# Optimization experiments

Measured on AMD Instinct MI355X. Metric: run time of the kernel, lower is better.

Reference implementation:

```python
import jax, jax.numpy as jnp
import numpy as np

B, S, D, H, DFF, L_ENC, L_DEC = 2, 1024, 512, 8, 2048, 2, 2
DK = D // H
NEG = -1e19


def _xavier(k, shape):
    a = jnp.sqrt(6.0 / (shape[-2] + shape[-1]))
    return jax.random.uniform(k, shape, minval=-a, maxval=a, dtype=jnp.float32)


def _kaiming(k, shape):
    return jax.random.normal(k, shape, dtype=jnp.float32) * jnp.sqrt(2.0 / shape[-2])


def setup_inputs():
    key = jax.random.key(0)
    ks = jax.random.split(key, 18)
    return {
        "X": jax.random.normal(ks[0], (B, S, D), dtype=jnp.float32),
        "output": jax.random.normal(ks[1], (B, S - 1, D), dtype=jnp.float32),
        "enc_qkv_comb": _xavier(ks[2], (L_ENC, 3, D, DK)),
        "enc_qkv_head": _xavier(ks[3], (L_ENC, 3, H, DK, DK)),
        "enc_WO": _xavier(ks[4], (L_ENC, H * DK, D)),
        "enc_bO": jnp.zeros((L_ENC, D), dtype=jnp.float32),
        "enc_W1": _kaiming(ks[5], (L_ENC, D, DFF)),
        "enc_W2": _kaiming(ks[6], (L_ENC, DFF, D)),
        "dec_self_qkv_comb": _xavier(ks[7], (L_DEC, 3, D, DK)),
        "dec_self_qkv_head": _xavier(ks[8], (L_DEC, 3, H, DK, DK)),
        "dec_self_WO": _xavier(ks[9], (L_DEC, H * DK, D)),
        "dec_self_bO": jnp.zeros((L_DEC, D), dtype=jnp.float32),
        "dec_cross_qkv_comb": _xavier(ks[10], (L_DEC, 3, D, DK)),
        "dec_cross_qkv_head": _xavier(ks[11], (L_DEC, 3, H, DK, DK)),
        "dec_cross_WO": _xavier(ks[12], (L_DEC, H * DK, D)),
        "dec_cross_bO": jnp.zeros((L_DEC, D), dtype=jnp.float32),
        "dec_W1": _kaiming(ks[13], (L_DEC, D, DFF)),
        "dec_W2": _kaiming(ks[14], (L_DEC, DFF, D)),
    }


def layer_norm(x):
    # NOTE: original normalizes over the BATCH dim (dim=0) with unbiased std
    mean = jnp.mean(x, axis=0)
    std = jnp.std(x, axis=0, ddof=1)
    return (x - mean) / (std + 1e-4)


def pos_encoding(x):
    s, d = x.shape[1], x.shape[2]
    pos = jnp.arange(s, dtype=jnp.float32)[:, None]
    div = jnp.power(10000.0, -jnp.arange(0, d, 2, dtype=jnp.float32) / d)
    pe = jnp.zeros((s, d), dtype=x.dtype)
    pe = pe.at[:, 0::2].set(jnp.sin(pos * div)).at[:, 1::2].set(jnp.cos(pos * div))
    return x + pe


def mha(xq, xk, xv, qkv_comb, qkv_head, WO, bO, pad_q, pad_k, causal, scale_after):
    # Q_i = XQ @ WQ_comb @ WQ[i]  (vectorized over heads)
    b, sq, _ = xq.shape
    Q = jnp.einsum('bsd,dk,hkj->bhsj', xq, qkv_comb[0], qkv_head[0])
    K = jnp.einsum('bsd,dk,hkj->bhsj', xk, qkv_comb[1], qkv_head[1])
    V = jnp.einsum('bsd,dk,hkj->bhsj', xv, qkv_comb[2], qkv_head[2])
    scores = jnp.einsum('bhqj,bhkj->bhqk', Q, K)
    add = jnp.where(pad_q[:, None, :, None] | pad_k[:, None, None, :], NEG, 0.0)
    inv = 1.0 / jnp.sqrt(jnp.float32(DK))
    if causal:
        sk = xk.shape[1]
        cm = jnp.where(jnp.tril(jnp.ones((sq, sk), dtype=jnp.float32)) == 0, NEG, 0.0)
        add = jnp.minimum(add, cm)
        # original masked attention: scale AFTER softmax, softmax over QUERY dim
        attn = jax.nn.softmax(scores + add, axis=2) * inv
    else:
        # original attention: softmax over QUERY dim (dim=1 of [B,Q,K])
        attn = jax.nn.softmax((scores + add) * inv, axis=2)
    out = jnp.einsum('bhqk,bhkj->bqhj', attn, V).reshape(b, sq, H * DK)
    return out @ WO + bO


def _forward(X, output, enc_qkv_comb, enc_qkv_head, enc_WO, enc_bO, enc_W1, enc_W2,
             dec_self_qkv_comb, dec_self_qkv_head, dec_self_WO, dec_self_bO,
             dec_cross_qkv_comb, dec_cross_qkv_head, dec_cross_WO, dec_cross_bO,
             dec_W1, dec_W2):
    gelu = lambda x: jax.nn.gelu(x, approximate=False)
    pad_in = jnp.all(X == 0, axis=-1)  # [B, S]
    cur = pos_encoding(X)  # identity embedding
    for i in range(L_ENC):
        n = layer_norm(cur)
        a = mha(n, n, n, enc_qkv_comb[i], enc_qkv_head[i], enc_WO[i], enc_bO[i],
                pad_in, pad_in, causal=False, scale_after=False)
        r = a + n
        an = layer_norm(r)
        cur = gelu(an @ enc_W1[i]) @ enc_W2[i] + an
    enc_repr = cur

    out = jnp.concatenate([jnp.ones((X.shape[0], 1, output.shape[2]), output.dtype), output], axis=1)
    pad_out = jnp.all(out == 0, axis=-1)  # [B, S]
    cur = pos_encoding(out)
    for i in range(L_DEC):
        n = layer_norm(cur)
        # original bug preserved: decoder self-attn uses the INPUT padding mask
        a = mha(n, n, n, dec_self_qkv_comb[i], dec_self_qkv_head[i], dec_self_WO[i],
                dec_self_bO[i], pad_in, pad_in, causal=True, scale_after=True)
        r = a + n
        n2 = layer_norm(r)
        a2 = mha(n2, enc_repr, enc_repr, dec_cross_qkv_comb[i], dec_cross_qkv_head[i],
                 dec_cross_WO[i], dec_cross_bO[i], pad_out, pad_in, causal=False, scale_after=False)
        r2 = a2 + n2
        an = layer_norm(r2)
        cur = gelu(an @ dec_W1[i]) @ dec_W2[i] + an
    res = jnp.where(pad_out[:, :, None], 0.0, cur)
    return res[:, 1:, :]


def reference(X, output, enc_qkv_comb, enc_qkv_head, enc_WO, enc_bO, enc_W1, enc_W2,
              dec_self_qkv_comb, dec_self_qkv_head, dec_self_WO, dec_self_bO,
              dec_cross_qkv_comb, dec_cross_qkv_head, dec_cross_WO, dec_cross_bO,
              dec_W1, dec_W2):
    return _forward(X, output, enc_qkv_comb, enc_qkv_head, enc_WO, enc_bO, enc_W1, enc_W2,
                    dec_self_qkv_comb, dec_self_qkv_head, dec_self_WO, dec_self_bO,
                    dec_cross_qkv_comb, dec_cross_qkv_head, dec_cross_WO, dec_cross_bO,
                    dec_W1, dec_W2)
```

## Files before the change

kernel.cpp:

```cpp
#include <hip/hip_runtime.h>
#include <cstdint>
#include <cstddef>

constexpr int cB = 2, cS = 1024, cD = 512, cH = 8, cDK = 64, cDFF = 2048;
constexpr int cBS = cB * cS;
constexpr float kNEG = -1e19f;


__device__ __forceinline__ float gelu_f(float x)
{
    return 0.5f * x * (1.0f + erff(x * 0.70710678118654752440f));
}

template<int BN, int MODE, bool GELU>
__global__ __launch_bounds__(256) void sgemm(
    const float* __restrict__ A, const float* __restrict__ B, float* __restrict__ C,
    const float* __restrict__ bias, const float* __restrict__ resid,
    int K, int KS, int G2, int lda, int ldb, int ldc,
    long long a1, long long a2, long long b1, long long b2,
    long long c1, long long c2, long long plane)
{
    constexpr int BM = 128, BK = 16;
    constexpr int AP = BM + 4, BP = BN + 4;
    constexpr int MN = BN / 16;
    __shared__ float As[BK][AP];
    __shared__ float Bs[BK][BP];

    const int z = blockIdx.z;
    const int kc = z % KS;
    const int zz = z / KS;
    const int g1 = zz / G2, g2 = zz % G2;
    const float* Ab = A + (long long)g1 * a1 + (long long)g2 * a2;
    const float* Bb = B + (long long)g1 * b1 + (long long)g2 * b2;
    float* Cb = C + (long long)g1 * c1 + (long long)g2 * c2 + (long long)kc * plane;
    const int klen = K / KS, kbase = kc * klen;
    const int m0 = blockIdx.y * BM, n0 = blockIdx.x * BN;
    const int t = threadIdx.x, tx = t & 15, ty = t >> 4;

    float acc[8][MN];
    #pragma unroll
    for (int i = 0; i < 8; ++i)
        #pragma unroll
        for (int j = 0; j < MN; ++j) acc[i][j] = 0.f;

    for (int k0 = kbase; k0 < kbase + klen; k0 += BK) {
        if (MODE == 1) {
            #pragma unroll
            for (int r = 0; r < 2; ++r) {
                const int c = r * 256 + t, kk = c >> 5, m4 = c & 31;
                *(float4*)&As[kk][m4 * 4] =
                    *(const float4*)&Ab[(long long)(k0 + kk) * lda + m0 + m4 * 4];
            }
        } else {
            #pragma unroll
            for (int r = 0; r < 2; ++r) {
                const int c = r * 256 + t, kq = c & 3, mm = c >> 2;
                float4 v = *(const float4*)&Ab[(long long)(m0 + mm) * lda + k0 + kq * 4];
                As[kq * 4 + 0][mm] = v.x; As[kq * 4 + 1][mm] = v.y;
                As[kq * 4 + 2][mm] = v.z; As[kq * 4 + 3][mm] = v.w;
            }
        }
        if (MODE == 2) {
            #pragma unroll
            for (int r = 0; r < BN / 64; ++r) {
                const int c = r * 256 + t, kq = c & 3, nn = c >> 2;
                float4 v = *(const float4*)&Bb[(long long)(n0 + nn) * ldb + k0 + kq * 4];
                Bs[kq * 4 + 0][nn] = v.x; Bs[kq * 4 + 1][nn] = v.y;
                Bs[kq * 4 + 2][nn] = v.z; Bs[kq * 4 + 3][nn] = v.w;
            }
        } else {
            #pragma unroll
            for (int r = 0; r < BN / 64; ++r) {
                const int c = r * 256 + t, n4 = c & (BN / 4 - 1), kk = c / (BN / 4);
                *(float4*)&Bs[kk][n4 * 4] =
                    *(const float4*)&Bb[(long long)(k0 + kk) * ldb + n0 + n4 * 4];
            }
        }
        __syncthreads();
        #pragma unroll
        for (int kk = 0; kk < BK; ++kk) {
            float a[8], b[MN];
            *(float4*)&a[0] = *(const float4*)&As[kk][ty * 8];
            *(float4*)&a[4] = *(const float4*)&As[kk][ty * 8 + 4];
            *(float4*)&b[0] = *(const float4*)&Bs[kk][tx * 4];
            if (MN == 8)
                *(float4*)&b[4] = *(const float4*)&Bs[kk][64 + tx * 4];
            #pragma unroll
            for (int i = 0; i < 8; ++i)
                #pragma unroll
                for (int j = 0; j < MN; ++j)
                    acc[i][j] = fmaf(a[i], b[j], acc[i][j]);
        }
        __syncthreads();
    }

    #pragma unroll
    for (int i = 0; i < 8; ++i) {
        const int row = m0 + ty * 8 + i;
        #pragma unroll
        for (int g = 0; g < MN / 4; ++g) {
            const int col = n0 + g * 64 + tx * 4;
            float4 v;
            v.x = acc[i][g * 4 + 0]; v.y = acc[i][g * 4 + 1];
            v.z = acc[i][g * 4 + 2]; v.w = acc[i][g * 4 + 3];
            if (bias) {
                v.x += bias[col + 0]; v.y += bias[col + 1];
                v.z += bias[col + 2]; v.w += bias[col + 3];
            }
            if (GELU) {
                v.x = gelu_f(v.x); v.y = gelu_f(v.y);
                v.z = gelu_f(v.z); v.w = gelu_f(v.w);
            }
            const long long idx = (long long)row * ldc + col;
            if (resid) {
                float4 rr = *(const float4*)&resid[idx];
                v.x += rr.x; v.y += rr.y; v.z += rr.z; v.w += rr.w;
            }
            *(float4*)&Cb[idx] = v;
        }
    }
}

template<bool GELU>
__global__ __launch_bounds__(256) void reduce_flat(
    const float* __restrict__ parts, float* __restrict__ out, long long n,
    int ks, long long plane, const float* __restrict__ bias, int ldcMask,
    const float* __restrict__ resid)
{
    const long long i = ((long long)blockIdx.x * 256 + threadIdx.x) * 4;
    if (i >= n) return;
    float4 s = {0.f, 0.f, 0.f, 0.f};
    for (int z = 0; z < ks; ++z) {
        float4 v = *(const float4*)&parts[(long long)z * plane + i];
        s.x += v.x; s.y += v.y; s.z += v.z; s.w += v.w;
    }
    if (bias) {
        const int col = (int)(i & ldcMask);
        s.x += bias[col + 0]; s.y += bias[col + 1];
        s.z += bias[col + 2]; s.w += bias[col + 3];
    }
    if (GELU) {
        s.x = gelu_f(s.x); s.y = gelu_f(s.y);
        s.z = gelu_f(s.z); s.w = gelu_f(s.w);
    }
    if (resid) {
        float4 rr = *(const float4*)&resid[i];
        s.x += rr.x; s.y += rr.y; s.z += rr.z; s.w += rr.w;
    }
    *(float4*)&out[i] = s;
}

__global__ __launch_bounds__(256) void reduce_scatter(
    const float* __restrict__ parts, float* __restrict__ out, long long n,
    int ks, long long plane, int logN, int maskN, int ldcOut, int colBase)
{
    const long long i = ((long long)blockIdx.x * 256 + threadIdx.x) * 4;
    if (i >= n) return;
    float4 s = {0.f, 0.f, 0.f, 0.f};
    for (int z = 0; z < ks; ++z) {
        float4 v = *(const float4*)&parts[(long long)z * plane + i];
        s.x += v.x; s.y += v.y; s.z += v.z; s.w += v.w;
    }
    const long long row = i >> logN;
    const int col = (int)(i & maskN);
    *(float4*)&out[row * ldcOut + colBase + col] = s;
}

__global__ __launch_bounds__(256) void wct_gemm(
    const float* __restrict__ ec, const float* __restrict__ eh,
    const float* __restrict__ dsc, const float* __restrict__ dsh,
    const float* __restrict__ dcc, const float* __restrict__ dch,
    float* __restrict__ Wc3)
{
    constexpr long long LWH = 3LL * 512 * 64;
    __shared__ float As[16][132];
    __shared__ float Bs[16][68];
    const int bid = blockIdx.x;
    const int mt = bid & 3;
    const int zp = bid >> 2;
    const int zi = zp / 24;
    const int ph = zp % 24;
    const int p = ph >> 3, h = ph & 7;
    const int l = zi & 1;
    const float* comb = (zi < 2) ? ec : (zi < 4) ? dsc : dcc;
    const float* head = (zi < 2) ? eh : (zi < 4) ? dsh : dch;
    const float* Ab = comb + l * LWH + (long long)p * 512 * 64 + mt * 128 * 64;
    const float* Bb = head + l * LWH + (long long)ph * 4096;
    float* Cb = Wc3 + (long long)zi * 512 * 1536 + (long long)mt * 128 * 1536 + p * 512 + h * 64;
    const int t = threadIdx.x, tx = t & 15, ty = t >> 4;

    float acc[8][4];
    #pragma unroll
    for (int i = 0; i < 8; ++i)
        #pragma unroll
        for (int j = 0; j < 4; ++j) acc[i][j] = 0.f;

    for (int k0 = 0; k0 < 64; k0 += 16) {
        #pragma unroll
        for (int r = 0; r < 2; ++r) {
            const int c = r * 256 + t, kq = c & 3, mm = c >> 2;
            float4 v = *(const float4*)&Ab[mm * 64 + k0 + kq * 4];
            As[kq * 4 + 0][mm] = v.x; As[kq * 4 + 1][mm] = v.y;
            As[kq * 4 + 2][mm] = v.z; As[kq * 4 + 3][mm] = v.w;
        }
        {
            const int n4 = t & 15, kk = t >> 4;
            *(float4*)&Bs[kk][n4 * 4] = *(const float4*)&Bb[(k0 + kk) * 64 + n4 * 4];
        }
        __syncthreads();
        #pragma unroll
        for (int kk = 0; kk < 16; ++kk) {
            float a[8];
            *(float4*)&a[0] = *(const float4*)&As[kk][ty * 8];
            *(float4*)&a[4] = *(const float4*)&As[kk][ty * 8 + 4];
            float4 b4 = *(const float4*)&Bs[kk][tx * 4];
            const float b[4] = {b4.x, b4.y, b4.z, b4.w};
            #pragma unroll
            for (int i = 0; i < 8; ++i)
                #pragma unroll
                for (int j = 0; j < 4; ++j)
                    acc[i][j] = fmaf(a[i], b[j], acc[i][j]);
        }
        __syncthreads();
    }
    #pragma unroll
    for (int i = 0; i < 8; ++i) {
        const int row = ty * 8 + i;
        float4 v;
        v.x = acc[i][0]; v.y = acc[i][1]; v.z = acc[i][2]; v.w = acc[i][3];
        *(float4*)&Cb[(long long)row * 1536 + tx * 4] = v;
    }
}

template<bool CAUSAL>
__global__ __launch_bounds__(256) void softmax_kernel(
    float* __restrict__ sc, const unsigned char* __restrict__ padq,
    const unsigned char* __restrict__ padk, float scale)
{
    const int r = blockIdx.x;
    const int k = r & (cS - 1);
    const int b = r / (cH * cS);
    float* row = sc + (long long)r * cS;
    const bool pk = padk[b * cS + k] != 0;
    const int tid = threadIdx.x;
    float4 v4 = reinterpret_cast<const float4*>(row)[tid];
    float vals[4] = {v4.x, v4.y, v4.z, v4.w};
    #pragma unroll
    for (int u = 0; u < 4; ++u) {
        const int q = tid * 4 + u;
        bool masked = pk || (padq[b * cS + q] != 0);
        if (CAUSAL) masked = masked || (q < k);
        float x = vals[u];
        if (masked) x += kNEG;
        if (!CAUSAL) x *= scale;
        vals[u] = x;
    }
    float m = fmaxf(fmaxf(vals[0], vals[1]), fmaxf(vals[2], vals[3]));
    #pragma unroll
    for (int off = 32; off > 0; off >>= 1) m = fmaxf(m, __shfl_down(m, off));
    __shared__ float red[8];
    if ((tid & 63) == 0) red[tid >> 6] = m;
    __syncthreads();
    const float rm = fmaxf(fmaxf(red[0], red[1]), fmaxf(red[2], red[3]));
    float e[4], s = 0.f;
    #pragma unroll
    for (int u = 0; u < 4; ++u) { e[u] = expf(vals[u] - rm); s += e[u]; }
    #pragma unroll
    for (int off = 32; off > 0; off >>= 1) s += __shfl_down(s, off);
    if ((tid & 63) == 0) red[4 + (tid >> 6)] = s;
    __syncthreads();
    float inv = 1.0f / (red[4] + red[5] + red[6] + red[7]);
    if (CAUSAL) inv *= scale;
    v4.x = e[0] * inv; v4.y = e[1] * inv; v4.z = e[2] * inv; v4.w = e[3] * inv;
    reinterpret_cast<float4*>(row)[tid] = v4;
}

__global__ __launch_bounds__(256) void ln_kernel(const float* __restrict__ x, float* __restrict__ out)
{
    const long long idx = ((long long)blockIdx.x * 256 + threadIdx.x) * 4;
    float4 x0 = *(const float4*)&x[idx];
    float4 x1 = *(const float4*)&x[idx + (long long)cS * cD];
    float4 o;
    {
        const float d0 = x0.x - x1.x; o.x = (0.5f * d0) / (fabsf(d0) * 0.70710678f + 1e-4f);
        const float d1 = x0.y - x1.y; o.y = (0.5f * d1) / (fabsf(d1) * 0.70710678f + 1e-4f);
        const float d2 = x0.z - x1.z; o.z = (0.5f * d2) / (fabsf(d2) * 0.70710678f + 1e-4f);
        const float d3 = x0.w - x1.w; o.w = (0.5f * d3) / (fabsf(d3) * 0.70710678f + 1e-4f);
    }
    *(float4*)&out[idx] = o;
    float4 n;
    n.x = -o.x; n.y = -o.y; n.z = -o.z; n.w = -o.w;
    *(float4*)&out[idx + (long long)cS * cD] = n;
}

__global__ __launch_bounds__(256) void pad_in_kernel(const float* __restrict__ X, unsigned char* __restrict__ pad)
{
    const int r = blockIdx.x;
    const float* row = X + (long long)r * cD;
    const int tid = threadIdx.x;
    const bool nz = (row[tid] != 0.f) | (row[tid + 256] != 0.f);
    unsigned long long w = __ballot(nz);
    __shared__ unsigned long long sh[4];
    if ((tid & 63) == 0) sh[tid >> 6] = w;
    __syncthreads();
    if (tid == 0) pad[r] = ((sh[0] | sh[1] | sh[2] | sh[3]) == 0ULL) ? 1 : 0;
}

__global__ __launch_bounds__(256) void pad_dec_kernel(const float* __restrict__ outp, unsigned char* __restrict__ pad)
{
    const int r = blockIdx.x;
    const int s = r & (cS - 1);
    const int b = r >> 10;
    if (s == 0) { if (threadIdx.x == 0) pad[r] = 0; return; }
    const float* row = outp + ((long long)b * (cS - 1) + (s - 1)) * cD;
    const int tid = threadIdx.x;
    const bool nz = (row[tid] != 0.f) | (row[tid + 256] != 0.f);
    unsigned long long w = __ballot(nz);
    __shared__ unsigned long long sh[4];
    if ((tid & 63) == 0) sh[tid >> 6] = w;
    __syncthreads();
    if (tid == 0) pad[r] = ((sh[0] | sh[1] | sh[2] | sh[3]) == 0ULL) ? 1 : 0;
}

__device__ __forceinline__ float pe_val(int s, int d)
{
    const int i2 = d & ~1;
    const float dv = powf(10000.0f, -(float)i2 / (float)cD);
    const float ang = (float)s * dv;
    return (d & 1) ? cosf(ang) : sinf(ang);
}

__global__ __launch_bounds__(256) void posenc_enc_kernel(const float* __restrict__ X, float* __restrict__ out)
{
    const int r = blockIdx.x;
    const int s = r & (cS - 1);
    const int tid = threadIdx.x;
    #pragma unroll
    for (int u = 0; u < 2; ++u) {
        const int d = tid + 256 * u;
        out[(long long)r * cD + d] = X[(long long)r * cD + d] + pe_val(s, d);
    }
}

__global__ __launch_bounds__(256) void posenc_dec_kernel(const float* __restrict__ outp, float* __restrict__ out)
{
    const int r = blockIdx.x;
    const int s = r & (cS - 1);
    const int b = r >> 10;
    const int tid = threadIdx.x;
    #pragma unroll
    for (int u = 0; u < 2; ++u) {
        const int d = tid + 256 * u;
        const float base = (s == 0) ? 1.0f : outp[((long long)b * (cS - 1) + (s - 1)) * cD + d];
        out[(long long)r * cD + d] = base + pe_val(s, d);
    }
}

__global__ __launch_bounds__(256) void final_kernel(const float* __restrict__ cur,
                                                    const unsigned char* __restrict__ pad,
                                                    float* __restrict__ out)
{
    const int r = blockIdx.x;
    const int b = r / (cS - 1);
    const int s = r - b * (cS - 1) + 1;
    const int tid = threadIdx.x;
    const bool p = pad[b * cS + s] != 0;
    #pragma unroll
    for (int u = 0; u < 2; ++u) {
        const int d = tid + 256 * u;
        out[(long long)r * cD + d] = p ? 0.0f : cur[((long long)b * cS + s) * cD + d];
    }
}

struct Ws {
    float *t0, *t1, *t2, *t3, *wc3a, *qkv, *att, *parts, *sc, *ffn;
    unsigned char *pin, *pout;
};

static void run_mha(hipStream_t st, const Ws& w, int mhaIdx,
                    const float* xq, const float* xkv,
                    const float* WO, const float* bO,
                    const unsigned char* padq, const unsigned char* padk,
                    bool causal, const float* resid, float* outR)
{
    const long long M1 = 1048576;
    const float* wc3 = w.wc3a + (long long)mhaIdx * 512 * 1536;
    if (xq == xkv) {
        sgemm<64, 0, false><<<dim3(24, 16, 1), 256, 0, st>>>(
            xq, wc3, w.qkv, nullptr, nullptr, 512, 1, 1, 512, 1536, 1536,
            0, 0, 0, 0, 0, 0, 0);
    } else {
        sgemm<64, 0, false><<<dim3(8, 16, 4), 256, 0, st>>>(
            xq, wc3, w.parts, nullptr, nullptr, 512, 4, 1, 512, 1536, 512,
            0, 0, 0, 0, 0, 0, M1);
        reduce_scatter<<<dim3(1024), 256, 0, st>>>(w.parts, w.qkv, M1, 4, M1, 9, 511, 1536, 0);
        sgemm<64, 0, false><<<dim3(16, 16, 2), 256, 0, st>>>(
            xkv, wc3 + 512, w.parts, nullptr, nullptr, 512, 2, 1, 512, 1536, 1024,
            0, 0, 0, 0, 0, 0, 2 * M1);
        reduce_scatter<<<dim3(2048), 256, 0, st>>>(w.parts, w.qkv, 2 * M1, 2, 2 * M1, 10, 1023, 1536, 512);
    }
    sgemm<128, 2, false><<<dim3(8, 8, 16), 256, 0, st>>>(
        w.qkv + 512, w.qkv, w.sc, nullptr, nullptr, 64, 1, 8, 1536, 1536, 1024,
        1024LL * 1536, 64, 1024LL * 1536, 64, 8 * M1, M1, 0);
    {
        dim3 g(cB * cH * cS), blk(256);
        if (causal) softmax_kernel<true><<<g, blk, 0, st>>>(w.sc, padq, padk, 0.125f);
        else        softmax_kernel<false><<<g, blk, 0, st>>>(w.sc, padq, padk, 0.125f);
    }
    sgemm<64, 1, false><<<dim3(1, 8, 64), 256, 0, st>>>(
        w.sc, w.qkv + 1024, w.parts, nullptr, nullptr, 1024, 4, 8, 1024, 1536, 512,
        8 * M1, M1, 1024LL * 1536, 64, 1024LL * 512, 64, M1);
    reduce_flat<false><<<dim3(1024), 256, 0, st>>>(w.parts, w.att, M1, 4, M1, nullptr, 0, nullptr);
    sgemm<64, 0, false><<<dim3(8, 16, 4), 256, 0, st>>>(
        w.att, WO, w.parts, nullptr, nullptr, 512, 4, 1, 512, 512, 512,
        0, 0, 0, 0, 0, 0, M1);
    reduce_flat<false><<<dim3(1024), 256, 0, st>>>(w.parts, outR, M1, 4, M1, bO, 511, resid);
}

extern "C" void kernel_launch(void* const* d_in, const int* in_sizes, int n_in,
                              void* d_out, int out_size, void* d_ws, size_t ws_size,
                              hipStream_t stream)
{
    const float* X       = (const float*)d_in[0];
    const float* outp    = (const float*)d_in[1];
    const float* e_comb  = (const float*)d_in[2];
    const float* e_head  = (const float*)d_in[3];
    const float* e_WO    = (const float*)d_in[4];
    const float* e_bO    = (const float*)d_in[5];
    const float* e_W1    = (const float*)d_in[6];
    const float* e_W2    = (const float*)d_in[7];
    const float* ds_comb = (const float*)d_in[8];
    const float* ds_head = (const float*)d_in[9];
    const float* ds_WO   = (const float*)d_in[10];
    const float* ds_bO   = (const float*)d_in[11];
    const float* dc_comb = (const float*)d_in[12];
    const float* dc_head = (const float*)d_in[13];
    const float* dc_WO   = (const float*)d_in[14];
    const float* dc_bO   = (const float*)d_in[15];
    const float* d_W1    = (const float*)d_in[16];
    const float* d_W2    = (const float*)d_in[17];
    float* Y = (float*)d_out;

    Ws w;
    float* p = (float*)d_ws;
    const long long M1 = 1048576;
    w.t0   = p; p += M1;
    w.t1   = p; p += M1;
    w.t2   = p; p += M1;
    w.t3   = p; p += M1;
    w.wc3a = p; p += 6LL * 512 * 1536;
    w.qkv  = p; p += 2048LL * 1536;
    w.att  = p; p += M1;
    w.parts= p; p += 4 * M1;
    w.sc   = p; p += 16LL * M1;
    w.ffn  = w.sc;
    w.pin  = (unsigned char*)p;
    w.pout = w.pin + cB * cS;

    pad_in_kernel <<<dim3(cB * cS), 256, 0, stream>>>(X, w.pin);
    pad_dec_kernel<<<dim3(cB * cS), 256, 0, stream>>>(outp, w.pout);
    posenc_enc_kernel<<<dim3(cB * cS), 256, 0, stream>>>(X, w.t0);
    posenc_dec_kernel<<<dim3(cB * cS), 256, 0, stream>>>(outp, w.t3);
    wct_gemm<<<dim3(576), 256, 0, stream>>>(e_comb, e_head, ds_comb, ds_head, dc_comb, dc_head, w.wc3a);

    const dim3 lnGrid(cS * cD / 1024);

    for (int i = 0; i < 2; ++i) {
        ln_kernel<<<lnGrid, 256, 0, stream>>>(w.t0, w.t1);
        run_mha(stream, w, i, w.t1, w.t1,
                e_WO + (long long)i * cD * cD, e_bO + i * cD,
                w.pin, w.pin, false, w.t1, w.t2);
        ln_kernel<<<lnGrid, 256, 0, stream>>>(w.t2, w.t1);
        sgemm<64, 0, true><<<dim3(32, 16, 1), 256, 0, stream>>>(
            w.t1, e_W1 + (long long)i * cD * cDFF, w.ffn, nullptr, nullptr,
            512, 1, 1, 512, 2048, 2048, 0, 0, 0, 0, 0, 0, 0);
        sgemm<64, 0, false><<<dim3(8, 16, 4), 256, 0, stream>>>(
            w.ffn, e_W2 + (long long)i * cDFF * cD, w.parts, nullptr, nullptr,
            2048, 4, 1, 2048, 512, 512, 0, 0, 0, 0, 0, 0, M1);
        reduce_flat<false><<<dim3(1024), 256, 0, stream>>>(w.parts, w.t0, M1, 4, M1, nullptr, 0, w.t1);
    }

    for (int i = 0; i < 2; ++i) {
        ln_kernel<<<lnGrid, 256, 0, stream>>>(w.t3, w.t1);
        run_mha(stream, w, 2 + i, w.t1, w.t1,
                ds_WO + (long long)i * cD * cD, ds_bO + i * cD,
                w.pin, w.pin, true, w.t1, w.t2);
        ln_kernel<<<lnGrid, 256, 0, stream>>>(w.t2, w.t1);
        run_mha(stream, w, 4 + i, w.t1, w.t0,
                dc_WO + (long long)i * cD * cD, dc_bO + i * cD,
                w.pout, w.pin, false, w.t1, w.t2);
        ln_kernel<<<lnGrid, 256, 0, stream>>>(w.t2, w.t1);
        sgemm<64, 0, true><<<dim3(32, 16, 1), 256, 0, stream>>>(
            w.t1, d_W1 + (long long)i * cD * cDFF, w.ffn, nullptr, nullptr,
            512, 1, 1, 512, 2048, 2048, 0, 0, 0, 0, 0, 0, 0);
        sgemm<64, 0, false><<<dim3(8, 16, 4), 256, 0, stream>>>(
            w.ffn, d_W2 + (long long)i * cDFF * cD, w.parts, nullptr, nullptr,
            2048, 4, 1, 2048, 512, 512, 0, 0, 0, 0, 0, 0, M1);
        reduce_flat<false><<<dim3(1024), 256, 0, stream>>>(w.parts, w.t3, M1, 4, M1, nullptr, 0, w.t1);
    }

    final_kernel<<<dim3(cB * (cS - 1)), 256, 0, stream>>>(w.t3, w.pout, Y);
}
```

Before: 1.873 ms.

## Fuse softmax normalization into PV GEMM and double-buffer sgemm shared tiles

```diff
diff --git a/kernel.cpp b/kernel.cpp
--- a/kernel.cpp
+++ b/kernel.cpp
@@ -12,10 +12,21 @@
     return 0.5f * x * (1.0f + erff(x * 0.70710678118654752440f));
 }
 
-template<int BN, int MODE, bool GELU>
+template<int PVF>
+__device__ __forceinline__ float pvf1(float x, bool masked, int q, int kabs, float rm, float riv)
+{
+    if (PVF == 2) masked = masked || (q < kabs);
+    if (masked) x += kNEG;
+    if (PVF == 1) x *= 0.125f;
+    return expf(x - rm) * riv;
+}
+
+template<int BN, int MODE, bool GELU, int PVF>
 __global__ __launch_bounds__(256) void sgemm(
     const float* __restrict__ A, const float* __restrict__ B, float* __restrict__ C,
     const float* __restrict__ bias, const float* __restrict__ resid,
+    const float* __restrict__ stats, const unsigned char* __restrict__ padq,
+    const unsigned char* __restrict__ padk,
     int K, int KS, int G2, int lda, int ldb, int ldc,
     long long a1, long long a2, long long b1, long long b2,
     long long c1, long long c2, long long plane)
@@ -23,8 +34,8 @@
     constexpr int BM = 128, BK = 16;
     constexpr int AP = BM + 4, BP = BN + 4;
     constexpr int MN = BN / 16;
-    __shared__ float As[BK][AP];
-    __shared__ float Bs[BK][BP];
+    __shared__ float As0[BK][AP], As1[BK][AP];
+    __shared__ float Bs0[BK][BP], Bs1[BK][BP];
 
     const int z = blockIdx.z;
     const int kc = z % KS;
@@ -33,9 +44,18 @@
     const float* Ab = A + (long long)g1 * a1 + (long long)g2 * a2;
     const float* Bb = B + (long long)g1 * b1 + (long long)g2 * b2;
     float* Cb = C + (long long)g1 * c1 + (long long)g2 * c2 + (long long)kc * plane;
-    const int klen = K / KS, kbase = kc * klen;
+    const int klen = K / KS, kbase = kc * klen, kend = kbase + klen;
     const int m0 = blockIdx.y * BM, n0 = blockIdx.x * BN;
     const int t = threadIdx.x, tx = t & 15, ty = t >> 4;
+
+    const float* stm = nullptr;
+    const unsigned char* pqB = nullptr;
+    const unsigned char* pkB = nullptr;
+    if (PVF) {
+        stm = stats + (long long)zz * 2048;
+        pqB = padq + (long long)g1 * cS;
+        pkB = padk + (long long)g1 * cS;
+    }
 
     float acc[8][MN];
     #pragma unroll
@@ -43,55 +63,118 @@
         #pragma unroll
         for (int j = 0; j < MN; ++j) acc[i][j] = 0.f;
 
-    for (int k0 = kbase; k0 < kbase + klen; k0 += BK) {
+    float4 rA0, rA1, rB[BN / 64];
+    float2 rst[2]; unsigned char rpk[2]; uchar4 rpq[2];
+
+    auto loadAB = [&](int k0) {
         if (MODE == 1) {
             #pragma unroll
-            for (int r = 0; r < 2; ++r) {
-                const int c = r * 256 + t, kk = c >> 5, m4 = c & 31;
-                *(float4*)&As[kk][m4 * 4] =
-                    *(const float4*)&Ab[(long long)(k0 + kk) * lda + m0 + m4 * 4];
+            for (int rr = 0; rr < 2; ++rr) {
+                const int c = rr * 256 + t, kk = c >> 5, m4 = c & 31;
+                float4 v = *(const float4*)&Ab[(long long)(k0 + kk) * lda + m0 + m4 * 4];
+                if (rr == 0) rA0 = v; else rA1 = v;
+                if (PVF) {
+                    const int kabs = k0 + kk;
+                    rst[rr] = *(const float2*)&stm[kabs * 2];
+                    rpk[rr] = pkB[kabs];
+                    rpq[rr] = *(const uchar4*)&pqB[m0 + m4 * 4];
+                }
             }
         } else {
             #pragma unroll
-            for (int r = 0; r < 2; ++r) {
-                const int c = r * 256 + t, kq = c & 3, mm = c >> 2;
+            for (int rr = 0; rr < 2; ++rr) {
+                const int c = rr * 256 + t, kq = c & 3, mm = c >> 2;
                 float4 v = *(const float4*)&Ab[(long long)(m0 + mm) * lda + k0 + kq * 4];
-                As[kq * 4 + 0][mm] = v.x; As[kq * 4 + 1][mm] = v.y;
-                As[kq * 4 + 2][mm] = v.z; As[kq * 4 + 3][mm] = v.w;
+                if (rr == 0) rA0 = v; else rA1 = v;
             }
         }
         if (MODE == 2) {
             #pragma unroll
-            for (int r = 0; r < BN / 64; ++r) {
-                const int c = r * 256 + t, kq = c & 3, nn = c >> 2;
-                float4 v = *(const float4*)&Bb[(long long)(n0 + nn) * ldb + k0 + kq * 4];
-                Bs[kq * 4 + 0][nn] = v.x; Bs[kq * 4 + 1][nn] = v.y;
-                Bs[kq * 4 + 2][nn] = v.z; Bs[kq * 4 + 3][nn] = v.w;
+            for (int rr = 0; rr < BN / 64; ++rr) {
+                const int c = rr * 256 + t, kq = c & 3, nn = c >> 2;
+                rB[rr] = *(const float4*)&Bb[(long long)(n0 + nn) * ldb + k0 + kq * 4];
             }
         } else {
             #pragma unroll
-            for (int r = 0; r < BN / 64; ++r) {
-                const int c = r * 256 + t, n4 = c & (BN / 4 - 1), kk = c / (BN / 4);
-                *(float4*)&Bs[kk][n4 * 4] =
-                    *(const float4*)&Bb[(long long)(k0 + kk) * ldb + n0 + n4 * 4];
-            }
-        }
-        __syncthreads();
+            for (int rr = 0; rr < BN / 64; ++rr) {
+                const int c = rr * 256 + t, n4 = c & (BN / 4 - 1), kk = c / (BN / 4);
+                rB[rr] = *(const float4*)&Bb[(long long)(k0 + kk) * ldb + n0 + n4 * 4];
+            }
+        }
+    };
+
+    auto writeAB = [&](float (*AS)[AP], float (*BS)[BP], int k0) {
+        if (MODE == 1) {
+            #pragma unroll
+            for (int rr = 0; rr < 2; ++rr) {
+                const int c = rr * 256 + t, kk = c >> 5, m4 = c & 31;
+                float4 v = (rr == 0) ? rA0 : rA1;
+                if (PVF) {
+                    const int kabs = k0 + kk, q0 = m0 + m4 * 4;
+                    const float rm = rst[rr].x, riv = rst[rr].y;
+                    const bool pk = rpk[rr] != 0;
+                    v.x = pvf1<PVF>(v.x, pk || rpq[rr].x, q0 + 0, kabs, rm, riv);
+                    v.y = pvf1<PVF>(v.y, pk || rpq[rr].y, q0 + 1, kabs, rm, riv);
+                    v.z = pvf1<PVF>(v.z, pk || rpq[rr].z, q0 + 2, kabs, rm, riv);
+                    v.w = pvf1<PVF>(v.w, pk || rpq[rr].w, q0 + 3, kabs, rm, riv);
+                }
+                *(float4*)&AS[kk][m4 * 4] = v;
+            }
+        } else {
+            #pragma unroll
+            for (int rr = 0; rr < 2; ++rr) {
+                const int c = rr * 256 + t, kq = c & 3, mm = c >> 2;
+                float4 v = (rr == 0) ? rA0 : rA1;
+                AS[kq * 4 + 0][mm] = v.x; AS[kq * 4 + 1][mm] = v.y;
+                AS[kq * 4 + 2][mm] = v.z; AS[kq * 4 + 3][mm] = v.w;
+            }
+        }
+        if (MODE == 2) {
+            #pragma unroll
+            for (int rr = 0; rr < BN / 64; ++rr) {
+                const int c = rr * 256 + t, kq = c & 3, nn = c >> 2;
+                float4 v = rB[rr];
+                BS[kq * 4 + 0][nn] = v.x; BS[kq * 4 + 1][nn] = v.y;
+                BS[kq * 4 + 2][nn] = v.z; BS[kq * 4 + 3][nn] = v.w;
+            }
+        } else {
+            #pragma unroll
+            for (int rr = 0; rr < BN / 64; ++rr) {
+                const int c = rr * 256 + t, n4 = c & (BN / 4 - 1);
+                *(float4*)&BS[c / (BN / 4)][n4 * 4] = rB[rr];
+            }
+        }
+    };
+
+    auto compute = [&](float (*AS)[AP], float (*BS)[BP]) {
         #pragma unroll
         for (int kk = 0; kk < BK; ++kk) {
             float a[8], b[MN];
-            *(float4*)&a[0] = *(const float4*)&As[kk][ty * 8];
-            *(float4*)&a[4] = *(const float4*)&As[kk][ty * 8 + 4];
-            *(float4*)&b[0] = *(const float4*)&Bs[kk][tx * 4];
+            *(float4*)&a[0] = *(const float4*)&AS[kk][ty * 8];
+            *(float4*)&a[4] = *(const float4*)&AS[kk][ty * 8 + 4];
+            *(float4*)&b[0] = *(const float4*)&BS[kk][tx * 4];
             if (MN == 8)
-                *(float4*)&b[4] = *(const float4*)&Bs[kk][64 + tx * 4];
+                *(float4*)&b[4] = *(const float4*)&BS[kk][64 + tx * 4];
             #pragma unroll
             for (int i = 0; i < 8; ++i)
                 #pragma unroll
                 for (int j = 0; j < MN; ++j)
                     acc[i][j] = fmaf(a[i], b[j], acc[i][j]);
         }
+    };
+
+    loadAB(kbase);
+    writeAB(As0, Bs0, kbase);
+    for (int k0 = kbase; k0 < kend; k0 += 2 * BK) {
+        loadAB(k0 + BK);
         __syncthreads();
+        compute(As0, Bs0);
+        writeAB(As1, Bs1, k0 + BK);
+        const bool more = (k0 + 2 * BK) < kend;
+        if (more) loadAB(k0 + 2 * BK);
+        __syncthreads();
+        compute(As1, Bs1);
+        if (more) writeAB(As0, Bs0, k0 + 2 * BK);
     }
 
     #pragma unroll
@@ -233,14 +316,14 @@
 }
 
 template<bool CAUSAL>
-__global__ __launch_bounds__(256) void softmax_kernel(
-    float* __restrict__ sc, const unsigned char* __restrict__ padq,
-    const unsigned char* __restrict__ padk, float scale)
+__global__ __launch_bounds__(256) void sstats_kernel(
+    const float* __restrict__ sc, const unsigned char* __restrict__ padq,
+    const unsigned char* __restrict__ padk, float scale, float* __restrict__ stats)
 {
     const int r = blockIdx.x;
     const int k = r & (cS - 1);
     const int b = r / (cH * cS);
-    float* row = sc + (long long)r * cS;
+    const float* row = sc + (long long)r * cS;
     const bool pk = padk[b * cS + k] != 0;
     const int tid = threadIdx.x;
     float4 v4 = reinterpret_cast<const float4*>(row)[tid];
@@ -269,10 +352,12 @@
     for (int off = 32; off > 0; off >>= 1) s += __shfl_down(s, off);
     if ((tid & 63) == 0) red[4 + (tid >> 6)] = s;
     __syncthreads();
-    float inv = 1.0f / (red[4] + red[5] + red[6] + red[7]);
-    if (CAUSAL) inv *= scale;
-    v4.x = e[0] * inv; v4.y = e[1] * inv; v4.z = e[2] * inv; v4.w = e[3] * inv;
-    reinterpret_cast<float4*>(row)[tid] = v4;
+    if (tid == 0) {
+        float inv = 1.0f / (red[4] + red[5] + red[6] + red[7]);
+        if (CAUSAL) inv *= scale;
+        stats[2 * r] = rm;
+        stats[2 * r + 1] = inv;
+    }
 }
 
 __global__ __launch_bounds__(256) void ln_kernel(const float* __restrict__ x, float* __restrict__ out)
@@ -373,7 +458,7 @@
 }
 
 struct Ws {
-    float *t0, *t1, *t2, *t3, *wc3a, *qkv, *att, *parts, *sc, *ffn;
+    float *t0, *t1, *t2, *t3, *wc3a, *qkv, *att, *parts, *sc, *ffn, *stats;
     unsigned char *pin, *pout;
 };
 
@@ -386,34 +471,43 @@
     const long long M1 = 1048576;
     const float* wc3 = w.wc3a + (long long)mhaIdx * 512 * 1536;
     if (xq == xkv) {
-        sgemm<64, 0, false><<<dim3(24, 16, 1), 256, 0, st>>>(
-            xq, wc3, w.qkv, nullptr, nullptr, 512, 1, 1, 512, 1536, 1536,
-            0, 0, 0, 0, 0, 0, 0);
+        sgemm<64, 0, false, 0><<<dim3(24, 16, 1), 256, 0, st>>>(
+            xq, wc3, w.qkv, nullptr, nullptr, nullptr, nullptr, nullptr,
+            512, 1, 1, 512, 1536, 1536, 0, 0, 0, 0, 0, 0, 0);
     } else {
-        sgemm<64, 0, false><<<dim3(8, 16, 4), 256, 0, st>>>(
-            xq, wc3, w.parts, nullptr, nullptr, 512, 4, 1, 512, 1536, 512,
-            0, 0, 0, 0, 0, 0, M1);
+        sgemm<64, 0, false, 0><<<dim3(8, 16, 4), 256, 0, st>>>(
+            xq, wc3, w.parts, nullptr, nullptr, nullptr, nullptr, nullptr,
+            512, 4, 1, 512, 1536, 512, 0, 0, 0, 0, 0, 0, M1);
         reduce_scatter<<<dim3(1024), 256, 0, st>>>(w.parts, w.qkv, M1, 4, M1, 9, 511, 1536, 0);
-        sgemm<64, 0, false><<<dim3(16, 16, 2), 256, 0, st>>>(
-            xkv, wc3 + 512, w.parts, nullptr, nullptr, 512, 2, 1, 512, 1536, 1024,
-            0, 0, 0, 0, 0, 0, 2 * M1);
+        sgemm<64, 0, false, 0><<<dim3(16, 16, 2), 256, 0, st>>>(
+            xkv, wc3 + 512, w.parts, nullptr, nullptr, nullptr, nullptr, nullptr,
+            512, 2, 1, 512, 1536, 1024, 0, 0, 0, 0, 0, 0, 2 * M1);
         reduce_scatter<<<dim3(2048), 256, 0, st>>>(w.parts, w.qkv, 2 * M1, 2, 2 * M1, 10, 1023, 1536, 512);
     }
-    sgemm<128, 2, false><<<dim3(8, 8, 16), 256, 0, st>>>(
-        w.qkv + 512, w.qkv, w.sc, nullptr, nullptr, 64, 1, 8, 1536, 1536, 1024,
+    sgemm<128, 2, false, 0><<<dim3(8, 8, 16), 256, 0, st>>>(
+        w.qkv + 512, w.qkv, w.sc, nullptr, nullptr, nullptr, nullptr, nullptr,
+        64, 1, 8, 1536, 1536, 1024,
         1024LL * 1536, 64, 1024LL * 1536, 64, 8 * M1, M1, 0);
     {
         dim3 g(cB * cH * cS), blk(256);
-        if (causal) softmax_kernel<true><<<g, blk, 0, st>>>(w.sc, padq, padk, 0.125f);
-        else        softmax_kernel<false><<<g, blk, 0, st>>>(w.sc, padq, padk, 0.125f);
-    }
-    sgemm<64, 1, false><<<dim3(1, 8, 64), 256, 0, st>>>(
-        w.sc, w.qkv + 1024, w.parts, nullptr, nullptr, 1024, 4, 8, 1024, 1536, 512,
-        8 * M1, M1, 1024LL * 1536, 64, 1024LL * 512, 64, M1);
+        if (causal) sstats_kernel<true><<<g, blk, 0, st>>>(w.sc, padq, padk, 0.125f, w.stats);
+        else        sstats_kernel<false><<<g, blk, 0, st>>>(w.sc, padq, padk, 0.125f, w.stats);
+    }
+    if (causal) {
+        sgemm<64, 1, false, 2><<<dim3(1, 8, 64), 256, 0, st>>>(
+            w.sc, w.qkv + 1024, w.parts, nullptr, nullptr, w.stats, padq, padk,
+            1024, 4, 8, 1024, 1536, 512,
+            8 * M1, M1, 1024LL * 1536, 64, 1024LL * 512, 64, M1);
+    } else {
+        sgemm<64, 1, false, 1><<<dim3(1, 8, 64), 256, 0, st>>>(
+            w.sc, w.qkv + 1024, w.parts, nullptr, nullptr, w.stats, padq, padk,
+            1024, 4, 8, 1024, 1536, 512,
+            8 * M1, M1, 1024LL * 1536, 64, 1024LL * 512, 64, M1);
+    }
     reduce_flat<false><<<dim3(1024), 256, 0, st>>>(w.parts, w.att, M1, 4, M1, nullptr, 0, nullptr);
-    sgemm<64, 0, false><<<dim3(8, 16, 4), 256, 0, st>>>(
-        w.att, WO, w.parts, nullptr, nullptr, 512, 4, 1, 512, 512, 512,
-        0, 0, 0, 0, 0, 0, M1);
+    sgemm<64, 0, false, 0><<<dim3(8, 16, 4), 256, 0, st>>>(
+        w.att, WO, w.parts, nullptr, nullptr, nullptr, nullptr, nullptr,
+        512, 4, 1, 512, 512, 512, 0, 0, 0, 0, 0, 0, M1);
     reduce_flat<false><<<dim3(1024), 256, 0, st>>>(w.parts, outR, M1, 4, M1, bO, 511, resid);
 }
 
@@ -454,6 +548,7 @@
     w.parts= p; p += 4 * M1;
     w.sc   = p; p += 16LL * M1;
     w.ffn  = w.sc;
+    w.stats= p; p += 2LL * cB * cH * cS;
     w.pin  = (unsigned char*)p;
     w.pout = w.pin + cB * cS;
 
@@ -471,11 +566,11 @@
                 e_WO + (long long)i * cD * cD, e_bO + i * cD,
                 w.pin, w.pin, false, w.t1, w.t2);
         ln_kernel<<<lnGrid, 256, 0, stream>>>(w.t2, w.t1);
-        sgemm<64, 0, true><<<dim3(32, 16, 1), 256, 0, stream>>>(
-            w.t1, e_W1 + (long long)i * cD * cDFF, w.ffn, nullptr, nullptr,
+        sgemm<64, 0, true, 0><<<dim3(32, 16, 1), 256, 0, stream>>>(
+            w.t1, e_W1 + (long long)i * cD * cDFF, w.ffn, nullptr, nullptr, nullptr, nullptr, nullptr,
             512, 1, 1, 512, 2048, 2048, 0, 0, 0, 0, 0, 0, 0);
-        sgemm<64, 0, false><<<dim3(8, 16, 4), 256, 0, stream>>>(
-            w.ffn, e_W2 + (long long)i * cDFF * cD, w.parts, nullptr, nullptr,
+        sgemm<64, 0, false, 0><<<dim3(8, 16, 4), 256, 0, stream>>>(
+            w.ffn, e_W2 + (long long)i * cDFF * cD, w.parts, nullptr, nullptr, nullptr, nullptr, nullptr,
             2048, 4, 1, 2048, 512, 512, 0, 0, 0, 0, 0, 0, M1);
         reduce_flat<false><<<dim3(1024), 256, 0, stream>>>(w.parts, w.t0, M1, 4, M1, nullptr, 0, w.t1);
     }
@@ -490,11 +585,11 @@
                 dc_WO + (long long)i * cD * cD, dc_bO + i * cD,
                 w.pout, w.pin, false, w.t1, w.t2);
         ln_kernel<<<lnGrid, 256, 0, stream>>>(w.t2, w.t1);
-        sgemm<64, 0, true><<<dim3(32, 16, 1), 256, 0, stream>>>(
-            w.t1, d_W1 + (long long)i * cD * cDFF, w.ffn, nullptr, nullptr,
+        sgemm<64, 0, true, 0><<<dim3(32, 16, 1), 256, 0, stream>>>(
+            w.t1, d_W1 + (long long)i * cD * cDFF, w.ffn, nullptr, nullptr, nullptr, nullptr, nullptr,
             512, 1, 1, 512, 2048, 2048, 0, 0, 0, 0, 0, 0, 0);
-        sgemm<64, 0, false><<<dim3(8, 16, 4), 256, 0, stream>>>(
-            w.ffn, d_W2 + (long long)i * cDFF * cD, w.parts, nullptr, nullptr,
+        sgemm<64, 0, false, 0><<<dim3(8, 16, 4), 256, 0, stream>>>(
+            w.ffn, d_W2 + (long long)i * cDFF * cD, w.parts, nullptr, nullptr, nullptr, nullptr, nullptr,
             2048, 4, 1, 2048, 512, 512, 0, 0, 0, 0, 0, 0, M1);
         reduce_flat<false><<<dim3(1024), 256, 0, stream>>>(w.parts, w.t3, M1, 4, M1, nullptr, 0, w.t1);
     }
```

Result: slower. 2.158 ms (+15.2%).

## Fuse softmax normalization into PV GEMM operand load via per-row stats

Applied to the files above, without the earlier changes.

```diff
diff --git a/kernel.cpp b/kernel.cpp
--- a/kernel.cpp
+++ b/kernel.cpp
@@ -12,17 +12,29 @@
     return 0.5f * x * (1.0f + erff(x * 0.70710678118654752440f));
 }
 
-template<int BN, int MODE, bool GELU>
+template<int PVF>
+__device__ __forceinline__ float pvf1(float x, bool masked, int q, int kabs, float rm, float riv)
+{
+    if (PVF == 2) masked = masked || (q < kabs);
+    if (masked) x += kNEG;
+    if (PVF == 1) x *= 0.125f;
+    return expf(x - rm) * riv;
+}
+
+template<int BM, int BN, int MODE, bool GELU, int PVF>
 __global__ __launch_bounds__(256) void sgemm(
     const float* __restrict__ A, const float* __restrict__ B, float* __restrict__ C,
     const float* __restrict__ bias, const float* __restrict__ resid,
+    const float* __restrict__ stats, const unsigned char* __restrict__ padq,
+    const unsigned char* __restrict__ padk,
     int K, int KS, int G2, int lda, int ldb, int ldc,
     long long a1, long long a2, long long b1, long long b2,
     long long c1, long long c2, long long plane)
 {
-    constexpr int BM = 128, BK = 16;
+    constexpr int BK = 16;
     constexpr int AP = BM + 4, BP = BN + 4;
-    constexpr int MN = BN / 16;
+    constexpr int MR = BM / 16;
+    constexpr int NR = BN / 16;
     __shared__ float As[BK][AP];
     __shared__ float Bs[BK][BP];
 
@@ -37,23 +49,43 @@
     const int m0 = blockIdx.y * BM, n0 = blockIdx.x * BN;
     const int t = threadIdx.x, tx = t & 15, ty = t >> 4;
 
-    float acc[8][MN];
-    #pragma unroll
-    for (int i = 0; i < 8; ++i)
+    const float* stm = nullptr;
+    const unsigned char* pqB = nullptr;
+    const unsigned char* pkB = nullptr;
+    if (PVF) {
+        stm = stats + (long long)zz * 2048;
+        pqB = padq + (long long)g1 * cS;
+        pkB = padk + (long long)g1 * cS;
+    }
+
+    float acc[MR][NR];
+    #pragma unroll
+    for (int i = 0; i < MR; ++i)
         #pragma unroll
-        for (int j = 0; j < MN; ++j) acc[i][j] = 0.f;
+        for (int j = 0; j < NR; ++j) acc[i][j] = 0.f;
 
     for (int k0 = kbase; k0 < kbase + klen; k0 += BK) {
         if (MODE == 1) {
             #pragma unroll
-            for (int r = 0; r < 2; ++r) {
-                const int c = r * 256 + t, kk = c >> 5, m4 = c & 31;
-                *(float4*)&As[kk][m4 * 4] =
-                    *(const float4*)&Ab[(long long)(k0 + kk) * lda + m0 + m4 * 4];
+            for (int r = 0; r < BM / 64; ++r) {
+                const int c = r * 256 + t;
+                const int kk = c / (BM / 4), m4 = c % (BM / 4);
+                float4 v = *(const float4*)&Ab[(long long)(k0 + kk) * lda + m0 + m4 * 4];
+                if (PVF) {
+                    const int kabs = k0 + kk, q0 = m0 + m4 * 4;
+                    const float2 st = *(const float2*)&stm[kabs * 2];
+                    const bool pk = pkB[kabs] != 0;
+                    const uchar4 pq = *(const uchar4*)&pqB[q0];
+                    v.x = pvf1<PVF>(v.x, pk || pq.x, q0 + 0, kabs, st.x, st.y);
+                    v.y = pvf1<PVF>(v.y, pk || pq.y, q0 + 1, kabs, st.x, st.y);
+                    v.z = pvf1<PVF>(v.z, pk || pq.z, q0 + 2, kabs, st.x, st.y);
+                    v.w = pvf1<PVF>(v.w, pk || pq.w, q0 + 3, kabs, st.x, st.y);
+                }
+                *(float4*)&As[kk][m4 * 4] = v;
             }
         } else {
             #pragma unroll
-            for (int r = 0; r < 2; ++r) {
+            for (int r = 0; r < BM / 64; ++r) {
                 const int c = r * 256 + t, kq = c & 3, mm = c >> 2;
                 float4 v = *(const float4*)&Ab[(long long)(m0 + mm) * lda + k0 + kq * 4];
                 As[kq * 4 + 0][mm] = v.x; As[kq * 4 + 1][mm] = v.y;
@@ -79,26 +111,27 @@
         __syncthreads();
         #pragma unroll
         for (int kk = 0; kk < BK; ++kk) {
-            float a[8], b[MN];
-            *(float4*)&a[0] = *(const float4*)&As[kk][ty * 8];
-            *(float4*)&a[4] = *(const float4*)&As[kk][ty * 8 + 4];
+            float a[MR], b[NR];
+            #pragma unroll
+            for (int g = 0; g < MR / 4; ++g)
+                *(float4*)&a[g * 4] = *(const float4*)&As[kk][ty * MR + g * 4];
             *(float4*)&b[0] = *(const float4*)&Bs[kk][tx * 4];
-            if (MN == 8)
+            if (NR == 8)
                 *(float4*)&b[4] = *(const float4*)&Bs[kk][64 + tx * 4];
             #pragma unroll
-            for (int i = 0; i < 8; ++i)
+            for (int i = 0; i < MR; ++i)
                 #pragma unroll
-                for (int j = 0; j < MN; ++j)
+                for (int j = 0; j < NR; ++j)
                     acc[i][j] = fmaf(a[i], b[j], acc[i][j]);
         }
         __syncthreads();
     }
 
     #pragma unroll
-    for (int i = 0; i < 8; ++i) {
-        const int row = m0 + ty * 8 + i;
+    for (int i = 0; i < MR; ++i) {
+        const int row = m0 + ty * MR + i;
         #pragma unroll
-        for (int g = 0; g < MN / 4; ++g) {
+        for (int g = 0; g < NR / 4; ++g) {
             const int col = n0 + g * 64 + tx * 4;
             float4 v;
             v.x = acc[i][g * 4 + 0]; v.y = acc[i][g * 4 + 1];
@@ -233,14 +266,14 @@
 }
 
 template<bool CAUSAL>
-__global__ __launch_bounds__(256) void softmax_kernel(
-    float* __restrict__ sc, const unsigned char* __restrict__ padq,
-    const unsigned char* __restrict__ padk, float scale)
+__global__ __launch_bounds__(256) void sstats_kernel(
+    const float* __restrict__ sc, const unsigned char* __restrict__ padq,
+    const unsigned char* __restrict__ padk, float scale, float* __restrict__ stats)
 {
     const int r = blockIdx.x;
     const int k = r & (cS - 1);
     const int b = r / (cH * cS);
-    float* row = sc + (long long)r * cS;
+    const float* row = sc + (long long)r * cS;
     const bool pk = padk[b * cS + k] != 0;
     const int tid = threadIdx.x;
     float4 v4 = reinterpret_cast<const float4*>(row)[tid];
@@ -269,10 +302,12 @@
     for (int off = 32; off > 0; off >>= 1) s += __shfl_down(s, off);
     if ((tid & 63) == 0) red[4 + (tid >> 6)] = s;
     __syncthreads();
-    float inv = 1.0f / (red[4] + red[5] + red[6] + red[7]);
-    if (CAUSAL) inv *= scale;
-    v4.x = e[0] * inv; v4.y = e[1] * inv; v4.z = e[2] * inv; v4.w = e[3] * inv;
-    reinterpret_cast<float4*>(row)[tid] = v4;
+    if (tid == 0) {
+        float inv = 1.0f / (red[4] + red[5] + red[6] + red[7]);
+        if (CAUSAL) inv *= scale;
+        stats[2 * r] = rm;
+        stats[2 * r + 1] = inv;
+    }
 }
 
 __global__ __launch_bounds__(256) void ln_kernel(const float* __restrict__ x, float* __restrict__ out)
@@ -373,7 +408,7 @@
 }
 
 struct Ws {
-    float *t0, *t1, *t2, *t3, *wc3a, *qkv, *att, *parts, *sc, *ffn;
+    float *t0, *t1, *t2, *t3, *wc3a, *qkv, *att, *parts, *sc, *ffn, *stats;
     unsigned char *pin, *pout;
 };
 
@@ -386,34 +421,43 @@
     const long long M1 = 1048576;
     const float* wc3 = w.wc3a + (long long)mhaIdx * 512 * 1536;
     if (xq == xkv) {
-        sgemm<64, 0, false><<<dim3(24, 16, 1), 256, 0, st>>>(
-            xq, wc3, w.qkv, nullptr, nullptr, 512, 1, 1, 512, 1536, 1536,
-            0, 0, 0, 0, 0, 0, 0);
+        sgemm<128, 64, 0, false, 0><<<dim3(24, 16, 1), 256, 0, st>>>(
+            xq, wc3, w.qkv, nullptr, nullptr, nullptr, nullptr, nullptr,
+            512, 1, 1, 512, 1536, 1536, 0, 0, 0, 0, 0, 0, 0);
     } else {
-        sgemm<64, 0, false><<<dim3(8, 16, 4), 256, 0, st>>>(
-            xq, wc3, w.parts, nullptr, nullptr, 512, 4, 1, 512, 1536, 512,
-            0, 0, 0, 0, 0, 0, M1);
+        sgemm<128, 64, 0, false, 0><<<dim3(8, 16, 4), 256, 0, st>>>(
+            xq, wc3, w.parts, nullptr, nullptr, nullptr, nullptr, nullptr,
+            512, 4, 1, 512, 1536, 512, 0, 0, 0, 0, 0, 0, M1);
         reduce_scatter<<<dim3(1024), 256, 0, st>>>(w.parts, w.qkv, M1, 4, M1, 9, 511, 1536, 0);
-        sgemm<64, 0, false><<<dim3(16, 16, 2), 256, 0, st>>>(
-            xkv, wc3 + 512, w.parts, nullptr, nullptr, 512, 2, 1, 512, 1536, 1024,
-            0, 0, 0, 0, 0, 0, 2 * M1);
+        sgemm<128, 64, 0, false, 0><<<dim3(16, 16, 2), 256, 0, st>>>(
+            xkv, wc3 + 512, w.parts, nullptr, nullptr, nullptr, nullptr, nullptr,
+            512, 2, 1, 512, 1536, 1024, 0, 0, 0, 0, 0, 0, 2 * M1);
         reduce_scatter<<<dim3(2048), 256, 0, st>>>(w.parts, w.qkv, 2 * M1, 2, 2 * M1, 10, 1023, 1536, 512);
     }
-    sgemm<128, 2, false><<<dim3(8, 8, 16), 256, 0, st>>>(
-        w.qkv + 512, w.qkv, w.sc, nullptr, nullptr, 64, 1, 8, 1536, 1536, 1024,
+    sgemm<128, 128, 2, false, 0><<<dim3(8, 8, 16), 256, 0, st>>>(
+        w.qkv + 512, w.qkv, w.sc, nullptr, nullptr, nullptr, nullptr, nullptr,
+        64, 1, 8, 1536, 1536, 1024,
         1024LL * 1536, 64, 1024LL * 1536, 64, 8 * M1, M1, 0);
     {
         dim3 g(cB * cH * cS), blk(256);
-        if (causal) softmax_kernel<true><<<g, blk, 0, st>>>(w.sc, padq, padk, 0.125f);
-        else        softmax_kernel<false><<<g, blk, 0, st>>>(w.sc, padq, padk, 0.125f);
-    }
-    sgemm<64, 1, false><<<dim3(1, 8, 64), 256, 0, st>>>(
-        w.sc, w.qkv + 1024, w.parts, nullptr, nullptr, 1024, 4, 8, 1024, 1536, 512,
-        8 * M1, M1, 1024LL * 1536, 64, 1024LL * 512, 64, M1);
+        if (causal) sstats_kernel<true><<<g, blk, 0, st>>>(w.sc, padq, padk, 0.125f, w.stats);
+        else        sstats_kernel<false><<<g, blk, 0, st>>>(w.sc, padq, padk, 0.125f, w.stats);
+    }
+    if (causal) {
+        sgemm<64, 64, 1, false, 2><<<dim3(1, 16, 64), 256, 0, st>>>(
+            w.sc, w.qkv + 1024, w.parts, nullptr, nullptr, w.stats, padq, padk,
+            1024, 4, 8, 1024, 1536, 512,
+            8 * M1, M1, 1024LL * 1536, 64, 1024LL * 512, 64, M1);
+    } else {
+        sgemm<64, 64, 1, false, 1><<<dim3(1, 16, 64), 256, 0, st>>>(
+            w.sc, w.qkv + 1024, w.parts, nullptr, nullptr, w.stats, padq, padk,
+            1024, 4, 8, 1024, 1536, 512,
+            8 * M1, M1, 1024LL * 1536, 64, 1024LL * 512, 64, M1);
+    }
     reduce_flat<false><<<dim3(1024), 256, 0, st>>>(w.parts, w.att, M1, 4, M1, nullptr, 0, nullptr);
-    sgemm<64, 0, false><<<dim3(8, 16, 4), 256, 0, st>>>(
-        w.att, WO, w.parts, nullptr, nullptr, 512, 4, 1, 512, 512, 512,
-        0, 0, 0, 0, 0, 0, M1);
+    sgemm<128, 64, 0, false, 0><<<dim3(8, 16, 4), 256, 0, st>>>(
+        w.att, WO, w.parts, nullptr, nullptr, nullptr, nullptr, nullptr,
+        512, 4, 1, 512, 512, 512, 0, 0, 0, 0, 0, 0, M1);
     reduce_flat<false><<<dim3(1024), 256, 0, st>>>(w.parts, outR, M1, 4, M1, bO, 511, resid);
 }
 
@@ -454,6 +498,7 @@
     w.parts= p; p += 4 * M1;
     w.sc   = p; p += 16LL * M1;
     w.ffn  = w.sc;
+    w.stats= p; p += 2LL * cB * cH * cS;
     w.pin  = (unsigned char*)p;
     w.pout = w.pin + cB * cS;
 
@@ -471,11 +516,11 @@
                 e_WO + (long long)i * cD * cD, e_bO + i * cD,
                 w.pin, w.pin, false, w.t1, w.t2);
         ln_kernel<<<lnGrid, 256, 0, stream>>>(w.t2, w.t1);
-        sgemm<64, 0, true><<<dim3(32, 16, 1), 256, 0, stream>>>(
-            w.t1, e_W1 + (long long)i * cD * cDFF, w.ffn, nullptr, nullptr,
+        sgemm<128, 64, 0, true, 0><<<dim3(32, 16, 1), 256, 0, stream>>>(
+            w.t1, e_W1 + (long long)i * cD * cDFF, w.ffn, nullptr, nullptr, nullptr, nullptr, nullptr,
             512, 1, 1, 512, 2048, 2048, 0, 0, 0, 0, 0, 0, 0);
-        sgemm<64, 0, false><<<dim3(8, 16, 4), 256, 0, stream>>>(
-            w.ffn, e_W2 + (long long)i * cDFF * cD, w.parts, nullptr, nullptr,
+        sgemm<128, 64, 0, false, 0><<<dim3(8, 16, 4), 256, 0, stream>>>(
+            w.ffn, e_W2 + (long long)i * cDFF * cD, w.parts, nullptr, nullptr, nullptr, nullptr, nullptr,
             2048, 4, 1, 2048, 512, 512, 0, 0, 0, 0, 0, 0, M1);
         reduce_flat<false><<<dim3(1024), 256, 0, stream>>>(w.parts, w.t0, M1, 4, M1, nullptr, 0, w.t1);
     }
@@ -490,11 +535,11 @@
                 dc_WO + (long long)i * cD * cD, dc_bO + i * cD,
                 w.pout, w.pin, false, w.t1, w.t2);
         ln_kernel<<<lnGrid, 256, 0, stream>>>(w.t2, w.t1);
-        sgemm<64, 0, true><<<dim3(32, 16, 1), 256, 0, stream>>>(
-            w.t1, d_W1 + (long long)i * cD * cDFF, w.ffn, nullptr, nullptr,
+        sgemm<128, 64, 0, true, 0><<<dim3(32, 16, 1), 256, 0, stream>>>(
+            w.t1, d_W1 + (long long)i * cD * cDFF, w.ffn, nullptr, nullptr, nullptr, nullptr, nullptr,
             512, 1, 1, 512, 2048, 2048, 0, 0, 0, 0, 0, 0, 0);
-        sgemm<64, 0, false><<<dim3(8, 16, 4), 256, 0, stream>>>(
-            w.ffn, d_W2 + (long long)i * cDFF * cD, w.parts, nullptr, nullptr,
+        sgemm<128, 64, 0, false, 0><<<dim3(8, 16, 4), 256, 0, stream>>>(
+            w.ffn, d_W2 + (long long)i * cDFF * cD, w.parts, nullptr, nullptr, nullptr, nullptr, nullptr,
             2048, 4, 1, 2048, 512, 512, 0, 0, 0, 0, 0, 0, M1);
         reduce_flat<false><<<dim3(1024), 256, 0, stream>>>(w.parts, w.t3, M1, 4, M1, nullptr, 0, w.t1);
     }
```

After: 1.815 ms. -3.1%, faster.
